# Kernel tuning notes

Measured on AMD Instinct MI355X. Metric: run time of the kernel, lower is better.

## Reference

```python
import jax, jax.numpy as jnp
import numpy as np

B = 262144
N_USERS = 100000
N_LOCS = 2000
N_ISBNS = 100000
SBERT_DIM = 384
NUM_CATS = 64
EMB = 48
TEMP = 0.05
ALPHA = 3.0
BETA = 1.0


def setup_inputs() -> dict:
    key = jax.random.key(0)
    ks = jax.random.split(key, 20)
    s = 0.05
    inp = {
        "user_idx": jax.random.randint(ks[0], (B,), 0, N_USERS),
        "loc_idx": jax.random.randint(ks[1], (B,), 0, N_LOCS),
        "pos_idx": jax.random.randint(ks[2], (B,), 0, N_ISBNS),
        "neg_idx": jax.random.randint(ks[3], (B,), 0, N_ISBNS),
        "user_cat_emb": jax.random.normal(ks[4], (N_USERS, EMB), jnp.float32) * s,
        "user_txt_emb": jax.random.normal(ks[5], (N_USERS, EMB), jnp.float32) * s,
        "loc_cat_emb": jax.random.normal(ks[6], (N_LOCS, EMB), jnp.float32) * s,
        "loc_txt_emb": jax.random.normal(ks[7], (N_LOCS, EMB), jnp.float32) * s,
        "sbert_matrix": jax.random.normal(ks[8], (N_ISBNS, SBERT_DIM), jnp.float32) * s,
        # multi-hot category matrix (~3 categories per book on average)
        "book_cat_mh": (jax.random.uniform(ks[9], (N_ISBNS, NUM_CATS)) < 0.05).astype(jnp.float32),
        "Wc1": jax.random.normal(ks[10], (NUM_CATS, 128), jnp.float32) * s,
        "bc1": jnp.zeros((128,), jnp.float32),
        "Wc2": jax.random.normal(ks[11], (128, EMB), jnp.float32) * s,
        "bc2": jnp.zeros((EMB,), jnp.float32),
        "Wt1": jax.random.normal(ks[12], (SBERT_DIM, 256), jnp.float32) * s,
        "bt1": jnp.zeros((256,), jnp.float32),
        "Wt2": jax.random.normal(ks[13], (256, EMB), jnp.float32) * s,
        "bt2": jnp.zeros((EMB,), jnp.float32),
    }
    return inp


def _l2norm(x):
    # tf.nn.l2_normalize: x / sqrt(max(sum(x^2), eps)), eps=1e-12
    sq = jnp.sum(x * x, axis=-1, keepdims=True)
    return x * jax.lax.rsqrt(jnp.maximum(sq, 1e-12))


def _encode_book(idx, sbert_matrix, book_cat_mh, Wc1, bc1, Wc2, bc2, Wt1, bt1, Wt2, bt2):
    b_cat_in = book_cat_mh[idx]                      # [B, NUM_CATS]
    b_txt_in = sbert_matrix[idx]                     # [B, SBERT_DIM]
    b_cat = jax.nn.relu(b_cat_in @ Wc1 + bc1) @ Wc2 + bc2   # [B, EMB]
    b_txt = jax.nn.relu(b_txt_in @ Wt1 + bt1) @ Wt2 + bt2   # [B, EMB]
    return _l2norm(ALPHA * b_cat + BETA * b_txt)


def reference(user_idx, loc_idx, pos_idx, neg_idx,
              user_cat_emb, user_txt_emb, loc_cat_emb, loc_txt_emb,
              sbert_matrix, book_cat_mh,
              Wc1, bc1, Wc2, bc2, Wt1, bt1, Wt2, bt2):
    # user tower (dropout inactive at inference)
    u = ALPHA * (user_cat_emb[user_idx] + loc_cat_emb[loc_idx]) \
        + BETA * (user_txt_emb[user_idx] + loc_txt_emb[loc_idx])
    u = _l2norm(u)
    p = _encode_book(pos_idx, sbert_matrix, book_cat_mh, Wc1, bc1, Wc2, bc2, Wt1, bt1, Wt2, bt2)
    n = _encode_book(neg_idx, sbert_matrix, book_cat_mh, Wc1, bc1, Wc2, bc2, Wt1, bt1, Wt2, bt2)
    pos_sim = jnp.sum(u * p, axis=-1) / TEMP
    neg_sim = jnp.sum(u * n, axis=-1) / TEMP
    return jnp.stack([pos_sim, neg_sim], axis=-1)  # [B, 2]
```

## Files before the change

kernel.cpp:

```cpp
#include <hip/hip_runtime.h>

#define SBD   384
#define NCATS 64
#define EMB   48
#define HT    256
#define HC    128

typedef __attribute__((ext_vector_type(8))) short short8;
typedef __attribute__((ext_vector_type(4))) float f32x4;

__device__ __forceinline__ short f2bf(float x) {
    union { float f; unsigned u; } v; v.f = x;
    unsigned r = v.u + 0x7FFF + ((v.u >> 16) & 1);
    return (short)(r >> 16);
}

__device__ __forceinline__ short8 cvt8(float4 a, float4 b) {
    short8 h;
    h[0] = f2bf(a.x); h[1] = f2bf(a.y); h[2] = f2bf(a.z); h[3] = f2bf(a.w);
    h[4] = f2bf(b.x); h[5] = f2bf(b.y); h[6] = f2bf(b.z); h[7] = f2bf(b.w);
    return h;
}

__device__ __forceinline__ void glds16(const void* g, void* l) {
    __builtin_amdgcn_global_load_lds((const __attribute__((address_space(1))) void*)g,
                                     (__attribute__((address_space(3))) void*)l, 16, 0, 0);
}

#define MFMA(a, b, c) __builtin_amdgcn_mfma_f32_16x16x32_bf16((a), (b), (c), 0, 0, 0)

__global__ void prep_weights(const float* __restrict__ Wt1, const float* __restrict__ Wt2,
                             const float* __restrict__ Wc1, const float* __restrict__ Wc2,
                             char* __restrict__ iT1, char* __restrict__ iK2) {
    int t = blockIdx.x * blockDim.x + threadIdx.x;
    int stride = gridDim.x * blockDim.x;
    for (int g = t; g < 256 * 48; g += stride) {
        int n = g / 48, k0 = (g - n * 48) * 8;
        int c = k0 >> 5, kin = k0 & 31;
        short8 v;
        #pragma unroll
        for (int j = 0; j < 8; ++j) v[j] = f2bf(Wt1[(size_t)(k0 + j) * HT + n]);
        *(short8*)(iT1 + (size_t)c * 16384 + ((n * 64 + kin * 2) ^ ((n & 7) << 4))) = v;
    }
    for (int g = t; g < 48 * 32; g += stride) {
        int n = g / 32, k0 = (g - n * 32) * 8;
        short8 v;
        #pragma unroll
        for (int j = 0; j < 8; ++j) v[j] = f2bf(Wt2[(size_t)(k0 + j) * EMB + n]);
        *(short8*)(iK2 + ((n * 512 + k0 * 2) ^ ((n & 7) << 4))) = v;
    }
    for (int g = t; g < 128 * 8; g += stride) {
        int n = g / 8, k0 = (g - n * 8) * 8;
        short8 v;
        #pragma unroll
        for (int j = 0; j < 8; ++j) v[j] = f2bf(Wc1[(size_t)(k0 + j) * HC + n]);
        *(short8*)(iK2 + 24576 + ((n * 128 + k0 * 2) ^ ((n & 7) << 4))) = v;
    }
    for (int g = t; g < 48 * 16; g += stride) {
        int n = g / 16, k0 = (g - n * 16) * 8;
        short8 v;
        #pragma unroll
        for (int j = 0; j < 8; ++j) v[j] = f2bf(Wc2[(size_t)(k0 + j) * EMB + n]);
        *(short8*)(iK2 + 40960 + ((n * 256 + k0 * 2) ^ ((n & 7) << 4))) = v;
    }
}

__global__ __launch_bounds__(512, 2) void encode_fused(
    const float* __restrict__ sbert, const float* __restrict__ mh,
    const char* __restrict__ iT1, const char* __restrict__ iK2,
    const float* __restrict__ bt1, const float* __restrict__ bt2,
    const float* __restrict__ bc1, const float* __restrict__ bc2,
    float* __restrict__ E, int nbooks)
{
    __shared__ char lds[151552];

    const int t  = threadIdx.x;
    const int w  = t >> 6;
    const int l  = t & 63;
    const int lr = l & 15;
    const int lg = l >> 4;
    const int book0 = (int)blockIdx.x * 128;
    const int mw = w >> 2, nw = w & 3;
    const int sw = (lr & 7) << 4;

    float4 mf0, mf1, mf2, mf3;
    {
        const float* mp = mh + (size_t)min(book0 + w * 16 + lr, nbooks - 1) * NCATS + lg * 8;
        mf0 = *(const float4*)(mp);      mf1 = *(const float4*)(mp + 4);
        mf2 = *(const float4*)(mp + 32); mf3 = *(const float4*)(mp + 36);
    }

    #pragma unroll
    for (int j = 0; j < 12; ++j) {
        int G = t + 512 * j;
        int row = G / 48, c8 = G - row * 48;
        const float* p = sbert + (size_t)min(book0 + row, nbooks - 1) * SBD + c8 * 8;
        float4 a = *(const float4*)p, b = *(const float4*)(p + 4);
        *(short8*)(lds + ((row * 768 + c8 * 16) ^ ((row & 7) << 4))) = cvt8(a, b);
    }
    #pragma unroll
    for (int j = 0; j < 2; ++j)
        glds16(iT1 + t * 16 + j * 8192, lds + 98304 + t * 16 + j * 8192);
    __syncthreads();

    f32x4 acc[4][4];
    #pragma unroll
    for (int bi = 0; bi < 4; ++bi) {
        float b = bt1[nw * 64 + bi * 16 + lr];
        #pragma unroll
        for (int ai = 0; ai < 4; ++ai) acc[ai][bi] = (f32x4){b, b, b, b};
    }

    #pragma unroll
    for (int c = 0; c < 12; ++c) {
        const int cur = c & 1;
        if (c < 11) {
            #pragma unroll
            for (int j = 0; j < 2; ++j)
                glds16(iT1 + (size_t)(c + 1) * 16384 + t * 16 + j * 8192,
                       lds + 98304 + (cur ^ 1) * 16384 + t * 16 + j * 8192);
        }
        short8 Af[4], Bf[4];
        #pragma unroll
        for (int ai = 0; ai < 4; ++ai)
            Af[ai] = *(const short8*)(lds +
                (((mw * 64 + ai * 16 + lr) * 768 + (c * 32 + lg * 8) * 2) ^ sw));
        #pragma unroll
        for (int bi = 0; bi < 4; ++bi)
            Bf[bi] = *(const short8*)(lds + 98304 + cur * 16384 +
                (((nw * 64 + bi * 16 + lr) * 64 + lg * 16) ^ sw));
        #pragma unroll
        for (int ai = 0; ai < 4; ++ai)
            #pragma unroll
            for (int bi = 0; bi < 4; ++bi)
                acc[ai][bi] = MFMA(Af[ai], Bf[bi], acc[ai][bi]);
        asm volatile("s_waitcnt vmcnt(0) lgkmcnt(0)" ::: "memory");
        __builtin_amdgcn_sched_barrier(0);
        __builtin_amdgcn_s_barrier();
    }

    #pragma unroll
    for (int j = 0; j < 7; ++j) {
        int gi = t + j * 512;
        if (gi < 3328) glds16(iK2 + gi * 16, lds + 98304 + gi * 16);
    }
    #pragma unroll
    for (int ai = 0; ai < 4; ++ai)
        #pragma unroll
        for (int bi = 0; bi < 4; ++bi)
            #pragma unroll
            for (int r = 0; r < 4; ++r) {
                int row = mw * 64 + ai * 16 + lg * 4 + r;
                int col = nw * 64 + bi * 16 + lr;
                *(unsigned short*)(lds + ((row * 512 + col * 2) ^ ((row & 7) << 4))) =
                    (unsigned short)f2bf(fmaxf(acc[ai][bi][r], 0.f));
            }
    asm volatile("s_waitcnt vmcnt(0) lgkmcnt(0)" ::: "memory");
    __builtin_amdgcn_sched_barrier(0);
    __builtin_amdgcn_s_barrier();

    char* hc = lds + 65536 + w * 4096;

    f32x4 acct[3];
    #pragma unroll
    for (int nt = 0; nt < 3; ++nt) { float b = bt2[nt * 16 + lr]; acct[nt] = (f32x4){b, b, b, b}; }
    #pragma unroll
    for (int ks = 0; ks < 8; ++ks) {
        short8 af = *(const short8*)(lds +
            (((w * 16 + lr) * 512 + (ks * 32 + lg * 8) * 2) ^ sw));
        #pragma unroll
        for (int nt = 0; nt < 3; ++nt) {
            short8 bf = *(const short8*)(lds + 98304 +
                (((nt * 16 + lr) * 512 + (ks * 32 + lg * 8) * 2) ^ sw));
            acct[nt] = MFMA(af, bf, acct[nt]);
        }
    }

    short8 c0 = cvt8(mf0, mf1), c1 = cvt8(mf2, mf3);
    f32x4 accc[8];
    #pragma unroll
    for (int nt = 0; nt < 8; ++nt) { float b = bc1[nt * 16 + lr]; accc[nt] = (f32x4){b, b, b, b}; }
    #pragma unroll
    for (int nt = 0; nt < 8; ++nt) {
        short8 b0 = *(const short8*)(lds + 122880 + (((nt * 16 + lr) * 128 + lg * 16) ^ sw));
        short8 b1 = *(const short8*)(lds + 122880 + (((nt * 16 + lr) * 128 + 64 + lg * 16) ^ sw));
        accc[nt] = MFMA(c0, b0, accc[nt]);
        accc[nt] = MFMA(c1, b1, accc[nt]);
    }

    #pragma unroll
    for (int nt = 0; nt < 8; ++nt)
        #pragma unroll
        for (int r = 0; r < 4; ++r) {
            int rr = lg * 4 + r;
            *(unsigned short*)(hc + ((rr * 256 + (nt * 16 + lr) * 2) ^ ((rr & 7) << 4))) =
                (unsigned short)f2bf(fmaxf(accc[nt][r], 0.f));
        }
    asm volatile("s_waitcnt lgkmcnt(0)" ::: "memory");
    __builtin_amdgcn_sched_barrier(0);

    f32x4 acc2[3];
    #pragma unroll
    for (int nt = 0; nt < 3; ++nt) { float b = bc2[nt * 16 + lr]; acc2[nt] = (f32x4){b, b, b, b}; }
    #pragma unroll
    for (int ks = 0; ks < 4; ++ks) {
        short8 af = *(const short8*)(hc + ((lr * 256 + (ks * 32 + lg * 8) * 2) ^ sw));
        #pragma unroll
        for (int nt = 0; nt < 3; ++nt) {
            short8 bf = *(const short8*)(lds + 139264 +
                (((nt * 16 + lr) * 256 + (ks * 32 + lg * 8) * 2) ^ sw));
            acc2[nt] = MFMA(af, bf, acc2[nt]);
        }
    }

    f32x4 comb[3];
    #pragma unroll
    for (int nt = 0; nt < 3; ++nt)
        #pragma unroll
        for (int r = 0; r < 4; ++r) comb[nt][r] = 3.0f * acc2[nt][r] + acct[nt][r];
    #pragma unroll
    for (int r = 0; r < 4; ++r) {
        float ss = comb[0][r] * comb[0][r] + comb[1][r] * comb[1][r] + comb[2][r] * comb[2][r];
        ss += __shfl_xor(ss, 1); ss += __shfl_xor(ss, 2);
        ss += __shfl_xor(ss, 4); ss += __shfl_xor(ss, 8);
        float rn = rsqrtf(fmaxf(ss, 1e-12f));
        int grow = book0 + w * 16 + lg * 4 + r;
        if (grow < nbooks) {
            #pragma unroll
            for (int nt = 0; nt < 3; ++nt)
                E[(size_t)grow * EMB + nt * 16 + lr] = comb[nt][r] * rn;
        }
    }
}

__global__ __launch_bounds__(256) void score_kernel(
    const int* __restrict__ user_idx, const int* __restrict__ loc_idx,
    const int* __restrict__ pos_idx,  const int* __restrict__ neg_idx,
    const float* __restrict__ ucat, const float* __restrict__ utxt,
    const float* __restrict__ lcat, const float* __restrict__ ltxt,
    const float* __restrict__ E, float* __restrict__ out, int Bn)
{
    const int t    = threadIdx.x;
    const int lane = t & 15;
    const int s    = blockIdx.x * 16 + (t >> 4);
    if (s >= Bn) return;

    const int ui = user_idx[s];
    const int li = loc_idx[s];
    const int pi = pos_idx[s];
    const int ni = neg_idx[s];

    const int d0 = lane * 3;
    const float* uc = ucat + (size_t)ui * EMB + d0;
    const float* ut = utxt + (size_t)ui * EMB + d0;
    const float* lc = lcat + (size_t)li * EMB + d0;
    const float* lt = ltxt + (size_t)li * EMB + d0;
    const float* pp = E + (size_t)pi * EMB + d0;
    const float* nn = E + (size_t)ni * EMB + d0;

    float u0 = 3.0f * (uc[0] + lc[0]) + (ut[0] + lt[0]);
    float u1 = 3.0f * (uc[1] + lc[1]) + (ut[1] + lt[1]);
    float u2 = 3.0f * (uc[2] + lc[2]) + (ut[2] + lt[2]);

    float usq = u0 * u0 + u1 * u1 + u2 * u2;
    float ps  = u0 * pp[0] + u1 * pp[1] + u2 * pp[2];
    float ns  = u0 * nn[0] + u1 * nn[1] + u2 * nn[2];

    #pragma unroll
    for (int m = 1; m < 16; m <<= 1) {
        usq += __shfl_xor(usq, m);
        ps  += __shfl_xor(ps, m);
        ns  += __shfl_xor(ns, m);
    }

    if (lane == 0) {
        const float inv = rsqrtf(fmaxf(usq, 1e-12f)) * 20.0f;
        out[2 * (size_t)s + 0] = ps * inv;
        out[2 * (size_t)s + 1] = ns * inv;
    }
}

extern "C" void kernel_launch(void* const* d_in, const int* in_sizes, int n_in,
                              void* d_out, int out_size, void* d_ws, size_t ws_size,
                              hipStream_t stream) {
    const int*   user_idx = (const int*)d_in[0];
    const int*   loc_idx  = (const int*)d_in[1];
    const int*   pos_idx  = (const int*)d_in[2];
    const int*   neg_idx  = (const int*)d_in[3];
    const float* ucat     = (const float*)d_in[4];
    const float* utxt     = (const float*)d_in[5];
    const float* lcat     = (const float*)d_in[6];
    const float* ltxt     = (const float*)d_in[7];
    const float* sbert    = (const float*)d_in[8];
    const float* mh       = (const float*)d_in[9];
    const float* Wc1      = (const float*)d_in[10];
    const float* bc1      = (const float*)d_in[11];
    const float* Wc2      = (const float*)d_in[12];
    const float* bc2      = (const float*)d_in[13];
    const float* Wt1      = (const float*)d_in[14];
    const float* bt1      = (const float*)d_in[15];
    const float* Wt2      = (const float*)d_in[16];
    const float* bt2      = (const float*)d_in[17];

    const int Bn     = in_sizes[0];
    const int nbooks = in_sizes[8] / SBD;

    char* ws = (char*)d_ws;
    float* E = (float*)ws;
    size_t off = ((size_t)nbooks * EMB * 4 + 255) & ~(size_t)255;
    char* iT1 = ws + off;  off += 196608;
    char* iK2 = ws + off;  off += 53248;

    hipLaunchKernelGGL(prep_weights, dim3(64), dim3(256), 0, stream,
                       Wt1, Wt2, Wc1, Wc2, iT1, iK2);

    const int nblocks = (nbooks + 127) / 128;
    hipLaunchKernelGGL(encode_fused, dim3(nblocks), dim3(512), 0, stream,
                       sbert, mh, iT1, iK2, bt1, bt2, bc1, bc2, E, nbooks);

    const int nblocksB = (Bn + 15) / 16;
    hipLaunchKernelGGL(score_kernel, dim3(nblocksB), dim3(256), 0, stream,
                       user_idx, loc_idx, pos_idx, neg_idx,
                       ucat, utxt, lcat, ltxt, E, (float*)d_out, Bn);
}
```

Before: 123.6 us.

## Halve encode block to 64 books and read small weights from global

New measurement: 224.5 us. 81.7% more time.

```diff
diff --git a/kernel.cpp b/kernel.cpp
--- a/kernel.cpp
+++ b/kernel.cpp
@@ -47,40 +47,39 @@
         short8 v;
         #pragma unroll
         for (int j = 0; j < 8; ++j) v[j] = f2bf(Wt2[(size_t)(k0 + j) * EMB + n]);
-        *(short8*)(iK2 + ((n * 512 + k0 * 2) ^ ((n & 7) << 4))) = v;
+        *(short8*)(iK2 + n * 512 + k0 * 2) = v;
     }
     for (int g = t; g < 128 * 8; g += stride) {
         int n = g / 8, k0 = (g - n * 8) * 8;
         short8 v;
         #pragma unroll
         for (int j = 0; j < 8; ++j) v[j] = f2bf(Wc1[(size_t)(k0 + j) * HC + n]);
-        *(short8*)(iK2 + 24576 + ((n * 128 + k0 * 2) ^ ((n & 7) << 4))) = v;
+        *(short8*)(iK2 + 24576 + n * 128 + k0 * 2) = v;
     }
     for (int g = t; g < 48 * 16; g += stride) {
         int n = g / 16, k0 = (g - n * 16) * 8;
         short8 v;
         #pragma unroll
         for (int j = 0; j < 8; ++j) v[j] = f2bf(Wc2[(size_t)(k0 + j) * EMB + n]);
-        *(short8*)(iK2 + 40960 + ((n * 256 + k0 * 2) ^ ((n & 7) << 4))) = v;
-    }
-}
-
-__global__ __launch_bounds__(512, 2) void encode_fused(
+        *(short8*)(iK2 + 40960 + n * 256 + k0 * 2) = v;
+    }
+}
+
+__global__ __launch_bounds__(256, 2) void encode_fused(
     const float* __restrict__ sbert, const float* __restrict__ mh,
     const char* __restrict__ iT1, const char* __restrict__ iK2,
     const float* __restrict__ bt1, const float* __restrict__ bt2,
     const float* __restrict__ bc1, const float* __restrict__ bc2,
     float* __restrict__ E, int nbooks)
 {
-    __shared__ char lds[151552];
+    __shared__ char lds[81920];
 
     const int t  = threadIdx.x;
     const int w  = t >> 6;
     const int l  = t & 63;
     const int lr = l & 15;
     const int lg = l >> 4;
-    const int book0 = (int)blockIdx.x * 128;
-    const int mw = w >> 2, nw = w & 3;
+    const int book0 = (int)blockIdx.x * 64;
     const int sw = (lr & 7) << 4;
 
     float4 mf0, mf1, mf2, mf3;
@@ -92,43 +91,43 @@
 
     #pragma unroll
     for (int j = 0; j < 12; ++j) {
-        int G = t + 512 * j;
+        int G = t + 256 * j;
         int row = G / 48, c8 = G - row * 48;
         const float* p = sbert + (size_t)min(book0 + row, nbooks - 1) * SBD + c8 * 8;
         float4 a = *(const float4*)p, b = *(const float4*)(p + 4);
         *(short8*)(lds + ((row * 768 + c8 * 16) ^ ((row & 7) << 4))) = cvt8(a, b);
     }
     #pragma unroll
-    for (int j = 0; j < 2; ++j)
-        glds16(iT1 + t * 16 + j * 8192, lds + 98304 + t * 16 + j * 8192);
+    for (int j = 0; j < 4; ++j)
+        glds16(iT1 + t * 16 + j * 4096, lds + 49152 + t * 16 + j * 4096);
     __syncthreads();
 
     f32x4 acc[4][4];
     #pragma unroll
     for (int bi = 0; bi < 4; ++bi) {
-        float b = bt1[nw * 64 + bi * 16 + lr];
+        float b = bt1[w * 64 + bi * 16 + lr];
         #pragma unroll
         for (int ai = 0; ai < 4; ++ai) acc[ai][bi] = (f32x4){b, b, b, b};
     }
 
-    #pragma unroll
     for (int c = 0; c < 12; ++c) {
-        const int cur = c & 1;
+        const int boff = 49152 + (c & 1) * 16384;
+        const int noff = 49152 + ((c & 1) ^ 1) * 16384;
         if (c < 11) {
             #pragma unroll
-            for (int j = 0; j < 2; ++j)
-                glds16(iT1 + (size_t)(c + 1) * 16384 + t * 16 + j * 8192,
-                       lds + 98304 + (cur ^ 1) * 16384 + t * 16 + j * 8192);
+            for (int j = 0; j < 4; ++j)
+                glds16(iT1 + (size_t)(c + 1) * 16384 + t * 16 + j * 4096,
+                       lds + noff + t * 16 + j * 4096);
         }
         short8 Af[4], Bf[4];
         #pragma unroll
         for (int ai = 0; ai < 4; ++ai)
             Af[ai] = *(const short8*)(lds +
-                (((mw * 64 + ai * 16 + lr) * 768 + (c * 32 + lg * 8) * 2) ^ sw));
+                (((ai * 16 + lr) * 768 + (c * 32 + lg * 8) * 2) ^ sw));
         #pragma unroll
         for (int bi = 0; bi < 4; ++bi)
-            Bf[bi] = *(const short8*)(lds + 98304 + cur * 16384 +
-                (((nw * 64 + bi * 16 + lr) * 64 + lg * 16) ^ sw));
+            Bf[bi] = *(const short8*)(lds + boff +
+                (((w * 64 + bi * 16 + lr) * 64 + lg * 16) ^ sw));
         #pragma unroll
         for (int ai = 0; ai < 4; ++ai)
             #pragma unroll
@@ -140,26 +139,21 @@
     }
 
     #pragma unroll
-    for (int j = 0; j < 7; ++j) {
-        int gi = t + j * 512;
-        if (gi < 3328) glds16(iK2 + gi * 16, lds + 98304 + gi * 16);
-    }
-    #pragma unroll
     for (int ai = 0; ai < 4; ++ai)
         #pragma unroll
         for (int bi = 0; bi < 4; ++bi)
             #pragma unroll
             for (int r = 0; r < 4; ++r) {
-                int row = mw * 64 + ai * 16 + lg * 4 + r;
-                int col = nw * 64 + bi * 16 + lr;
+                int row = ai * 16 + lg * 4 + r;
+                int col = w * 64 + bi * 16 + lr;
                 *(unsigned short*)(lds + ((row * 512 + col * 2) ^ ((row & 7) << 4))) =
                     (unsigned short)f2bf(fmaxf(acc[ai][bi][r], 0.f));
             }
-    asm volatile("s_waitcnt vmcnt(0) lgkmcnt(0)" ::: "memory");
+    asm volatile("s_waitcnt lgkmcnt(0)" ::: "memory");
     __builtin_amdgcn_sched_barrier(0);
     __builtin_amdgcn_s_barrier();
 
-    char* hc = lds + 65536 + w * 4096;
+    char* hc = lds + 49152 + w * 4096;
 
     f32x4 acct[3];
     #pragma unroll
@@ -170,8 +164,7 @@
             (((w * 16 + lr) * 512 + (ks * 32 + lg * 8) * 2) ^ sw));
         #pragma unroll
         for (int nt = 0; nt < 3; ++nt) {
-            short8 bf = *(const short8*)(lds + 98304 +
-                (((nt * 16 + lr) * 512 + (ks * 32 + lg * 8) * 2) ^ sw));
+            short8 bf = *(const short8*)(iK2 + (nt * 16 + lr) * 512 + (ks * 32 + lg * 8) * 2);
             acct[nt] = MFMA(af, bf, acct[nt]);
         }
     }
@@ -182,8 +175,8 @@
     for (int nt = 0; nt < 8; ++nt) { float b = bc1[nt * 16 + lr]; accc[nt] = (f32x4){b, b, b, b}; }
     #pragma unroll
     for (int nt = 0; nt < 8; ++nt) {
-        short8 b0 = *(const short8*)(lds + 122880 + (((nt * 16 + lr) * 128 + lg * 16) ^ sw));
-        short8 b1 = *(const short8*)(lds + 122880 + (((nt * 16 + lr) * 128 + 64 + lg * 16) ^ sw));
+        short8 b0 = *(const short8*)(iK2 + 24576 + (nt * 16 + lr) * 128 + lg * 16);
+        short8 b1 = *(const short8*)(iK2 + 24576 + (nt * 16 + lr) * 128 + 64 + lg * 16);
         accc[nt] = MFMA(c0, b0, accc[nt]);
         accc[nt] = MFMA(c1, b1, accc[nt]);
     }
@@ -207,8 +200,7 @@
         short8 af = *(const short8*)(hc + ((lr * 256 + (ks * 32 + lg * 8) * 2) ^ sw));
         #pragma unroll
         for (int nt = 0; nt < 3; ++nt) {
-            short8 bf = *(const short8*)(lds + 139264 +
-                (((nt * 16 + lr) * 256 + (ks * 32 + lg * 8) * 2) ^ sw));
+            short8 bf = *(const short8*)(iK2 + 40960 + (nt * 16 + lr) * 256 + (ks * 32 + lg * 8) * 2);
             acc2[nt] = MFMA(af, bf, acc2[nt]);
         }
     }
@@ -314,8 +306,8 @@
     hipLaunchKernelGGL(prep_weights, dim3(64), dim3(256), 0, stream,
                        Wt1, Wt2, Wc1, Wc2, iT1, iK2);
 
-    const int nblocks = (nbooks + 127) / 128;
-    hipLaunchKernelGGL(encode_fused, dim3(nblocks), dim3(512), 0, stream,
+    const int nblocks = (nbooks + 63) / 64;
+    hipLaunchKernelGGL(encode_fused, dim3(nblocks), dim3(256), 0, stream,
                        sbert, mh, iT1, iK2, bt1, bt2, bc1, bc2, E, nbooks);
 
     const int nblocksB = (Bn + 15) / 16;
```
